# Kernel optimization log

Measured on AMD Instinct MI355X. Metric: run time of the kernel, lower is better.

Reference implementation:

```python
import jax, jax.numpy as jnp
import numpy as np

N_CANONICAL = 16
D_IN, D_HID, D_OUT = 784, 128, 10
BATCH = 65536


def setup_inputs() -> dict:
    key = jax.random.key(0)
    ks = jax.random.split(key, 6)
    x = jax.random.normal(ks[0], (BATCH, D_IN), dtype=jnp.float32)
    # per-canonical Linear params (PyTorch Linear: y = x @ W.T + b)
    s1 = 1.0 / np.sqrt(D_IN)
    s2 = 1.0 / np.sqrt(D_HID)
    fc_w = jax.random.uniform(ks[1], (N_CANONICAL, D_HID, D_IN), jnp.float32, -s1, s1)
    fc_b = jax.random.uniform(ks[2], (N_CANONICAL, D_HID), jnp.float32, -s1, s1)
    cls_w = jax.random.uniform(ks[3], (N_CANONICAL, D_OUT, D_HID), jnp.float32, -s2, s2)
    cls_b = jax.random.uniform(ks[4], (N_CANONICAL, D_OUT), jnp.float32, -s2, s2)
    factor = jnp.full((N_CANONICAL,), 1.0 / N_CANONICAL, dtype=jnp.float32)
    return {"x": x, "fc_w": fc_w, "fc_b": fc_b, "cls_w": cls_w, "cls_b": cls_b, "factor": factor}


def reference(x, fc_w, fc_b, cls_w, cls_b, factor):
    # x: [B, 784] (already flattened view of 28x28)
    # Ensemble of Linears combined by learned scalar factor. Since the combination
    # is linear, pre-combine weights: sum_k factor[k] * W_k (same math, fused GEMM).
    w1 = jnp.einsum('k,kod->od', factor, fc_w)   # [128, 784]
    b1 = factor @ fc_b                           # [128]
    h = jax.nn.relu(x @ w1.T + b1)               # [B, 128]
    w2 = jnp.einsum('k,kod->od', factor, cls_w)  # [10, 128]
    b2 = factor @ cls_b                          # [10]
    out = h @ w2.T + b2                          # [B, 10]
    return out
```

## Files before the change

### kernel.cpp

```cpp
#include <hip/hip_runtime.h>
#include <hip/hip_bf16.h>

typedef __attribute__((ext_vector_type(8))) short short8;
typedef __attribute__((ext_vector_type(4))) float f32x4;

#define N_ENS 16
#define D_IN 784
#define D_HID 128
#define D_OUT 10
#define KPAD 800
#define NKT 25
#define TILE_B 8192
#define WS_B1 204800
#define WS_W2 205312
#define WS_B2 210432

__device__ __forceinline__ unsigned short f2bf(float f) {
  unsigned int u = __float_as_uint(f);
  return (unsigned short)((u + 0x7FFFu + ((u >> 16) & 1u)) >> 16);
}

__device__ __forceinline__ void gload_lds16(const void* g, void* l) {
  __builtin_amdgcn_global_load_lds((const __attribute__((address_space(1))) void*)g,
                                   (__attribute__((address_space(3))) void*)l, 16, 0, 0);
}

__global__ void prep_kernel(const float* __restrict__ fc_w, const float* __restrict__ fc_b,
                            const float* __restrict__ cls_w, const float* __restrict__ cls_b,
                            const float* __restrict__ factor, char* __restrict__ ws) {
  int tid = blockIdx.x * 256 + threadIdx.x;
  float f[N_ENS];
#pragma unroll
  for (int e = 0; e < N_ENS; ++e) f[e] = factor[e];

  if (tid < D_HID * KPAD) {
    int col = tid / KPAD;
    int k   = tid - col * KPAD;
    float v = 0.f;
    if (k < D_IN) {
#pragma unroll
      for (int e = 0; e < N_ENS; ++e) v += f[e] * fc_w[(size_t)(e * D_HID + col) * D_IN + k];
    }
    int kt = k >> 5, kk = k & 31;
    int byte = kt * TILE_B + col * 64 + ((kk >> 3) << 4) + ((kk & 7) << 1);
    *(unsigned short*)(ws + byte) = f2bf(v);
  } else if (tid < D_HID * KPAD + D_HID) {
    int col = tid - D_HID * KPAD;
    float v = 0.f;
#pragma unroll
    for (int e = 0; e < N_ENS; ++e) v += f[e] * fc_b[e * D_HID + col];
    *(float*)(ws + WS_B1 + col * 4) = v;
  } else if (tid < D_HID * KPAD + D_HID + D_HID * D_OUT) {
    int i = tid - (D_HID * KPAD + D_HID);
    int o = i >> 7, n = i & 127;
    float v = 0.f;
#pragma unroll
    for (int e = 0; e < N_ENS; ++e) v += f[e] * cls_w[(e * D_OUT + o) * D_HID + n];
    *(float*)(ws + WS_W2 + i * 4) = v;
  } else if (tid < D_HID * KPAD + D_HID + D_HID * D_OUT + D_OUT) {
    int o = tid - (D_HID * KPAD + D_HID + D_HID * D_OUT);
    float v = 0.f;
#pragma unroll
    for (int e = 0; e < N_ENS; ++e) v += f[e] * cls_b[e * D_OUT + o];
    *(float*)(ws + WS_B2 + o * 4) = v;
  }
}

__global__ __launch_bounds__(256, 4) void mnist_fused(const float* __restrict__ x,
                                                      const char* __restrict__ ws,
                                                      float* __restrict__ out) {
  __shared__ __align__(16) char smem[38912];
  const int tid  = threadIdx.x;
  const int lane = tid & 63;
  const int w    = tid >> 6;
  const int l15  = lane & 15;
  const int kg   = lane >> 4;
  const int m0   = blockIdx.x * 64;

  const float* ar = x + (size_t)(m0 + w * 16 + l15) * D_IN;
  const int bfrag = l15 * 64 + kg * 16;

  f32x4 acc[8];
#pragma unroll
  for (int ni = 0; ni < 8; ++ni) acc[ni] = f32x4{0.f, 0.f, 0.f, 0.f};

  gload_lds16(ws + w * 2048 + lane * 16,        smem + w * 2048);
  gload_lds16(ws + w * 2048 + 1024 + lane * 16, smem + w * 2048 + 1024);
  float4 a0 = *(const float4*)(ar + kg * 8);
  float4 a1 = *(const float4*)(ar + kg * 8 + 4);

  for (int kt = 0; kt < NKT; ++kt) {
    const int cur = kt & 1;
    const int ktn = kt + 1;
    if (ktn < NKT) {
      const char* src = ws + ktn * TILE_B + w * 2048;
      char* dst = smem + (ktn & 1) * 8192 + w * 2048;
      gload_lds16(src + lane * 16, dst);
      gload_lds16(src + 1024 + lane * 16, dst + 1024);
    }
    union { unsigned short u[8]; short8 s; } pk;
    pk.u[0] = f2bf(a0.x); pk.u[1] = f2bf(a0.y); pk.u[2] = f2bf(a0.z); pk.u[3] = f2bf(a0.w);
    pk.u[4] = f2bf(a1.x); pk.u[5] = f2bf(a1.y); pk.u[6] = f2bf(a1.z); pk.u[7] = f2bf(a1.w);
    if (ktn < NKT) {
      if (ktn < 24 || kg < 2) {
        a0 = *(const float4*)(ar + ktn * 32 + kg * 8);
        a1 = *(const float4*)(ar + ktn * 32 + kg * 8 + 4);
      } else {
        a0 = float4{0.f, 0.f, 0.f, 0.f};
        a1 = float4{0.f, 0.f, 0.f, 0.f};
      }
      __builtin_amdgcn_sched_barrier(0);
      asm volatile("s_waitcnt vmcnt(4)" ::: "memory");
      __builtin_amdgcn_sched_barrier(0);
    } else {
      __builtin_amdgcn_sched_barrier(0);
      asm volatile("s_waitcnt vmcnt(0)" ::: "memory");
      __builtin_amdgcn_sched_barrier(0);
    }
    __builtin_amdgcn_s_barrier();
    __builtin_amdgcn_sched_barrier(0);
    {
      const char* Bb = smem + cur * 8192 + bfrag;
      short8 b[8];
#pragma unroll
      for (int ni = 0; ni < 8; ++ni) b[ni] = *(const short8*)(Bb + ni * 1024);
#pragma unroll
      for (int ni = 0; ni < 8; ++ni)
        acc[ni] = __builtin_amdgcn_mfma_f32_16x16x32_bf16(pk.s, b[ni], acc[ni], 0, 0, 0);
    }
    __builtin_amdgcn_sched_barrier(0);
    __builtin_amdgcn_s_barrier();
    __builtin_amdgcn_sched_barrier(0);
  }

  const float* b1g = (const float*)(ws + WS_B1);
  float (*h)[132] = (float (*)[132])smem;
#pragma unroll
  for (int ni = 0; ni < 8; ++ni) {
    const float bv = b1g[ni * 16 + l15];
#pragma unroll
    for (int j = 0; j < 4; ++j) {
      float v = acc[ni][j] + bv;
      h[w * 16 + kg * 4 + j][ni * 16 + l15] = v > 0.f ? v : 0.f;
    }
  }
  float* w2s = (float*)(smem + 33792);
  {
    const float* w2g = (const float*)(ws + WS_W2);
    for (int i = tid; i < 1280; i += 256) w2s[i] = w2g[i];
  }
  __syncthreads();

  const int row = w * 16 + l15;
  float po[10];
#pragma unroll
  for (int o = 0; o < 10; ++o) po[o] = 0.f;
#pragma unroll
  for (int n4 = 0; n4 < 8; ++n4) {
    const float4 hv = *(const float4*)(&h[row][kg * 32 + n4 * 4]);
#pragma unroll
    for (int o = 0; o < 10; ++o) {
      const float4 wv = *(const float4*)(w2s + o * 128 + kg * 32 + n4 * 4);
      po[o] += hv.x * wv.x + hv.y * wv.y + hv.z * wv.z + hv.w * wv.w;
    }
  }
#pragma unroll
  for (int o = 0; o < 10; ++o) {
    po[o] += __shfl_xor(po[o], 16);
    po[o] += __shfl_xor(po[o], 32);
  }
  if (kg == 0) {
    const float* b2g = (const float*)(ws + WS_B2);
    float* op = out + (size_t)(m0 + row) * 10;
#pragma unroll
    for (int o = 0; o < 10; o += 2) {
      float2 v;
      v.x = po[o]     + b2g[o];
      v.y = po[o + 1] + b2g[o + 1];
      *(float2*)(op + o) = v;
    }
  }
}

extern "C" void kernel_launch(void* const* d_in, const int* in_sizes, int n_in,
                              void* d_out, int out_size, void* d_ws, size_t ws_size,
                              hipStream_t stream) {
  const float* x      = (const float*)d_in[0];
  const float* fc_w   = (const float*)d_in[1];
  const float* fc_b   = (const float*)d_in[2];
  const float* cls_w  = (const float*)d_in[3];
  const float* cls_b  = (const float*)d_in[4];
  const float* factor = (const float*)d_in[5];
  char* ws = (char*)d_ws;
  float* outp = (float*)d_out;

  prep_kernel<<<406, 256, 0, stream>>>(fc_w, fc_b, cls_w, cls_b, factor, ws);
  mnist_fused<<<1024, 256, 0, stream>>>(x, ws, outp);
}
```

Before: 49.24 us.

## Swizzle LDS weight tile layout and vectorize weight-combine prep kernel

Introduces an XOR swizzle for the bf16 weight tile so each lane's 16-byte B-fragment reads from LDS spread across banks instead of conflicting at a 64-byte column stride. The prep kernel now has each thread combine four consecutive k values with float4 loads and write them packed into the swizzled layout, cutting the thread count and launch size. A __syncthreads is added before the LDS buffer is reused for the hidden activations. Per-lane offsets are precomputed into registers, which adds a little register pressure.

```diff
diff --git a/kernel.cpp b/kernel.cpp
--- a/kernel.cpp
+++ b/kernel.cpp
@@ -25,6 +25,10 @@
                                    (__attribute__((address_space(3))) void*)l, 16, 0, 0);
 }
 
+__device__ __forceinline__ int bswz(int c, int kg) {
+  return ((c >> 1) << 7) + (((((c & 1) << 2) | kg) ^ ((c >> 1) & 7)) << 4);
+}
+
 __global__ void prep_kernel(const float* __restrict__ fc_w, const float* __restrict__ fc_b,
                             const float* __restrict__ cls_w, const float* __restrict__ cls_b,
                             const float* __restrict__ factor, char* __restrict__ ws) {
@@ -33,32 +37,37 @@
 #pragma unroll
   for (int e = 0; e < N_ENS; ++e) f[e] = factor[e];
 
-  if (tid < D_HID * KPAD) {
-    int col = tid / KPAD;
-    int k   = tid - col * KPAD;
-    float v = 0.f;
-    if (k < D_IN) {
-#pragma unroll
-      for (int e = 0; e < N_ENS; ++e) v += f[e] * fc_w[(size_t)(e * D_HID + col) * D_IN + k];
-    }
-    int kt = k >> 5, kk = k & 31;
-    int byte = kt * TILE_B + col * 64 + ((kk >> 3) << 4) + ((kk & 7) << 1);
-    *(unsigned short*)(ws + byte) = f2bf(v);
-  } else if (tid < D_HID * KPAD + D_HID) {
-    int col = tid - D_HID * KPAD;
+  if (tid < 25600) {
+    int col = tid / 200;
+    int kq  = tid - col * 200;
+    int k   = kq * 4;
+    float4 v = float4{0.f, 0.f, 0.f, 0.f};
+    if (k + 3 < D_IN) {
+#pragma unroll
+      for (int e = 0; e < N_ENS; ++e) {
+        const float4 t = *(const float4*)(fc_w + (size_t)(e * D_HID + col) * D_IN + k);
+        v.x += f[e] * t.x; v.y += f[e] * t.y; v.z += f[e] * t.z; v.w += f[e] * t.w;
+      }
+    }
+    const int kt = k >> 5, kg = (k & 31) >> 3, half = k & 7;
+    union { unsigned short u[4]; uint2 p; } pk;
+    pk.u[0] = f2bf(v.x); pk.u[1] = f2bf(v.y); pk.u[2] = f2bf(v.z); pk.u[3] = f2bf(v.w);
+    *(uint2*)(ws + kt * TILE_B + bswz(col, kg) + half * 2) = pk.p;
+  } else if (tid < 25600 + D_HID) {
+    int col = tid - 25600;
     float v = 0.f;
 #pragma unroll
     for (int e = 0; e < N_ENS; ++e) v += f[e] * fc_b[e * D_HID + col];
     *(float*)(ws + WS_B1 + col * 4) = v;
-  } else if (tid < D_HID * KPAD + D_HID + D_HID * D_OUT) {
-    int i = tid - (D_HID * KPAD + D_HID);
+  } else if (tid < 25600 + D_HID + D_HID * D_OUT) {
+    int i = tid - (25600 + D_HID);
     int o = i >> 7, n = i & 127;
     float v = 0.f;
 #pragma unroll
     for (int e = 0; e < N_ENS; ++e) v += f[e] * cls_w[(e * D_OUT + o) * D_HID + n];
     *(float*)(ws + WS_W2 + i * 4) = v;
-  } else if (tid < D_HID * KPAD + D_HID + D_HID * D_OUT + D_OUT) {
-    int o = tid - (D_HID * KPAD + D_HID + D_HID * D_OUT);
+  } else if (tid < 25600 + D_HID + D_HID * D_OUT + D_OUT) {
+    int o = tid - (25600 + D_HID + D_HID * D_OUT);
     float v = 0.f;
 #pragma unroll
     for (int e = 0; e < N_ENS; ++e) v += f[e] * cls_b[e * D_OUT + o];
@@ -78,7 +87,9 @@
   const int m0   = blockIdx.x * 64;
 
   const float* ar = x + (size_t)(m0 + w * 16 + l15) * D_IN;
-  const int bfrag = l15 * 64 + kg * 16;
+  int boff[8];
+#pragma unroll
+  for (int ni = 0; ni < 8; ++ni) boff[ni] = bswz(ni * 16 + l15, kg);
 
   f32x4 acc[8];
 #pragma unroll
@@ -120,10 +131,10 @@
     __builtin_amdgcn_s_barrier();
     __builtin_amdgcn_sched_barrier(0);
     {
-      const char* Bb = smem + cur * 8192 + bfrag;
+      const char* Bb = smem + cur * 8192;
       short8 b[8];
 #pragma unroll
-      for (int ni = 0; ni < 8; ++ni) b[ni] = *(const short8*)(Bb + ni * 1024);
+      for (int ni = 0; ni < 8; ++ni) b[ni] = *(const short8*)(Bb + boff[ni]);
 #pragma unroll
       for (int ni = 0; ni < 8; ++ni)
         acc[ni] = __builtin_amdgcn_mfma_f32_16x16x32_bf16(pk.s, b[ni], acc[ni], 0, 0, 0);
@@ -132,6 +143,8 @@
     __builtin_amdgcn_s_barrier();
     __builtin_amdgcn_sched_barrier(0);
   }
+
+  __syncthreads();
 
   const float* b1g = (const float*)(ws + WS_B1);
   float (*h)[132] = (float (*)[132])smem;
@@ -194,6 +207,6 @@
   char* ws = (char*)d_ws;
   float* outp = (float*)d_out;
 
-  prep_kernel<<<406, 256, 0, stream>>>(fc_w, fc_b, cls_w, cls_b, factor, ws);
+  prep_kernel<<<106, 256, 0, stream>>>(fc_w, fc_b, cls_w, cls_b, factor, ws);
   mnist_fused<<<1024, 256, 0, stream>>>(x, ws, outp);
 }
```

After: 49.37 us. No clear change (+0.3%).
